# Performance work log

Hardware: AMD Instinct MI355X
Metric: run time of the kernel (lower is better)

## Reference

```python
import jax, jax.numpy as jnp
import numpy as np

H, W = 120, 160
FX, FY = 572.4114, 573.57043
CX, CY = 325.2611, 242.04899
CHUNK = 1200  # 19200 / 1200 = 16 scan steps
W_EDGE = 5.0
INV_SQRT_2PI = 1.0 / np.sqrt(2.0 * np.pi)


def backproject(depth):
    # depth: [H, W] -> organized cloud [H, W, 3]
    x = (jnp.arange(W, dtype=depth.dtype) - CX)[None, :]
    y = (jnp.arange(H, dtype=depth.dtype) - CY)[:, None]
    return jnp.stack((x * depth / FX, y * depth / FY, depth), axis=2)


def min_sq_dists(a, b):
    # For each point in a [N,3], squared distance to nearest point in b [M,3].
    # Tiled (flash-style) min-reduction: never materializes the full NxM matrix.
    b2 = jnp.sum(b * b, axis=-1)  # [M]
    n = a.shape[0]
    a_chunks = a.reshape(n // CHUNK, CHUNK, 3)

    def step(_, ac):
        a2 = jnp.sum(ac * ac, axis=-1)  # [chunk]
        d = a2[:, None] + b2[None, :] - 2.0 * (ac @ b.T)  # [chunk, M]
        return None, jnp.min(jnp.maximum(d, 0.0), axis=1)

    _, mins = jax.lax.scan(step, None, a_chunks)
    return mins.reshape(n)


def dilate(mask, ksize=9):
    # torch: clamp(conv2d(mask, ones(k,k), padding=k//2), 0, 1)
    k = jnp.ones((1, 1, ksize, ksize), mask.dtype)
    pad = ksize // 2
    out = jax.lax.conv_general_dilated(
        mask, k, window_strides=(1, 1), padding=[(pad, pad), (pad, pad)],
        dimension_numbers=("NCHW", "OIHW", "NCHW"))
    return jnp.clip(out, 0.0, 1.0)


def compute_mask_edge_weights(mask):
    # NOTE: original code calls mask_dilate_torch for BOTH dilate and erode
    # (a bug in the source), so mask_edge == 0 everywhere; replicated faithfully.
    dilated = dilate(mask, 9)
    eroded = dilate(mask, 9)
    mask_edge = dilated - eroded
    return jnp.exp(-0.5 * (mask_edge * W_EDGE) ** 2) * INV_SQRT_2PI + 1.0


def weighted_ex_loss_probs(probs, target, weight):
    pos = target > 0
    neg = target == 0
    p = jnp.clip(probs, 1e-7, 1.0 - 1e-7)
    pos_loss = jnp.where(pos, -target * jnp.log(p) * weight, 0.0)
    neg_loss = jnp.where(neg, -jnp.log(1.0 - p) * weight, 0.0)
    num_pos = jnp.sum(pos)
    num_neg = jnp.sum(neg)
    loss = jnp.where(num_pos > 0, jnp.sum(pos_loss) / jnp.maximum(num_pos, 1), 0.0)
    loss = loss + jnp.where(num_neg > 0, jnp.sum(neg_loss) / jnp.maximum(num_neg, 1), 0.0)
    return loss


def setup_inputs() -> dict:
    key = jax.random.key(0)
    k1, k2, k3, k4 = jax.random.split(key, 4)
    pred_PM = jax.random.uniform(k1, (1, H, W), dtype=jnp.float32)
    pred_Ms = (jax.random.uniform(k2, (1, H, W)) > 0.5).astype(jnp.float32)
    # strictly positive depths so the depth>0 mask keeps all H*W points (static shapes)
    depth_src = jax.random.uniform(k3, (H, W), dtype=jnp.float32) * 2.0 + 0.1
    depth_tgt = jax.random.uniform(k4, (H, W), dtype=jnp.float32) * 2.0 + 0.1
    return {"pred_PM": pred_PM, "pred_Ms": pred_Ms,
            "depth_src": depth_src, "depth_tgt": depth_tgt}


def reference(pred_PM, pred_Ms, depth_src, depth_tgt):
    # chamfer loss: backproject both depths, symmetric NN squared distance
    src_pts = backproject(depth_src).reshape(-1, 3)  # all z>0 by construction
    tgt_pts = backproject(depth_tgt).reshape(-1, 3)
    cham_loss = jnp.mean(min_sq_dists(src_pts, tgt_pts)) + jnp.mean(min_sq_dists(tgt_pts, src_pts))
    # mask loss: edge-weighted BCE-style loss
    p = pred_PM.reshape(-1, 1, H, W)
    m = pred_Ms.reshape(-1, 1, H, W)
    weights = compute_mask_edge_weights(m)
    mask_loss = weighted_ex_loss_probs(p, m, weights)
    return (cham_loss, mask_loss)
```

## Files before the change

### kernel.cpp

```cpp
#include <hip/hip_runtime.h>
#include <math.h>

#define HH 120
#define WW 160
#define NPTS (HH * WW)
#define FXC 572.4114f
#define FYC 573.57043f
#define CXC 325.2611f
#define CYC 242.04899f

#define CH_BT   64
#define CH_T    10
#define CH_APB  (CH_BT * CH_T)
#define CH_ABLK (NPTS / CH_APB)
#define CH_BTILE 192
#define CH_SCH  (NPTS / CH_BTILE)

#define MASK_WGT 1.3989422804014327f

#define GB_CH 64
#define GB_MK 16
#define GB_TOT (GB_CH + GB_MK)
#define CH_SEG (2 * NPTS / GB_CH)
#define MK_SEG (NPTS / GB_MK)

__device__ __forceinline__ void backproject_pt(int idx, float d,
                                               float& px, float& py, float& pz) {
    int y = idx / WW;
    int x = idx - y * WW;
    px = ((float)x - CXC) * d * (1.0f / FXC);
    py = ((float)y - CYC) * d * (1.0f / FYC);
    pz = d;
}

__device__ __forceinline__ float min3f(float a, float b, float c) {
    float d;
    asm("v_min3_f32 %0, %1, %2, %3" : "=v"(d) : "v"(a), "v"(b), "v"(c));
    return d;
}

__global__ void __launch_bounds__(256) init_k(int* __restrict__ mins,
                                              int* __restrict__ accs) {
    int i = blockIdx.x * 256 + threadIdx.x;
    if (i < 2 * NPTS) mins[i] = 0x7F800000;
    if (i < 6) accs[i] = 0;
}

__global__ void __launch_bounds__(CH_BT, 6) chamfer_partial_k(
    const float* __restrict__ depth_src, const float* __restrict__ depth_tgt,
    int* __restrict__ mins_base) {
    const float* dA;
    const float* dB;
    int* mins;
    if (blockIdx.z == 0) { dA = depth_src; dB = depth_tgt; mins = mins_base; }
    else                 { dA = depth_tgt; dB = depth_src; mins = mins_base + NPTS; }

    __shared__ float4 bp[CH_BTILE];

    const int tid = threadIdx.x;
    const int ablk = blockIdx.x;
    const int s = blockIdx.y;

#pragma unroll
    for (int r = 0; r < CH_BTILE / CH_BT; ++r) {
        int jj = r * CH_BT + tid;
        int j = s * CH_BTILE + jj;
        float d = dB[j];
        float px, py, pz;
        backproject_pt(j, d, px, py, pz);
        bp[jj] = make_float4(2.0f * px, 2.0f * py, 2.0f * pz,
                             fmaf(px, px, fmaf(py, py, pz * pz)));
    }

    float nax[CH_T], nay[CH_T], naz[CH_T], mn[CH_T];
#pragma unroll
    for (int t = 0; t < CH_T; ++t) {
        int i = ablk * CH_APB + t * CH_BT + tid;
        float d = dA[i];
        float px, py, pz;
        backproject_pt(i, d, px, py, pz);
        nax[t] = -px; nay[t] = -py; naz[t] = -pz;
        mn[t] = INFINITY;
    }

    __syncthreads();

    for (int jj = 0; jj < CH_BTILE; jj += 2) {
        float4 q0 = bp[jj + 0];
        float4 q1 = bp[jj + 1];
#pragma unroll
        for (int t = 0; t < CH_T; ++t) {
            float r0 = fmaf(nax[t], q0.x, fmaf(nay[t], q0.y, fmaf(naz[t], q0.z, q0.w)));
            float r1 = fmaf(nax[t], q1.x, fmaf(nay[t], q1.y, fmaf(naz[t], q1.z, q1.w)));
            mn[t] = min3f(mn[t], r0, r1);
        }
    }

#pragma unroll
    for (int t = 0; t < CH_T; ++t) {
        int i = ablk * CH_APB + t * CH_BT + tid;
        float a2 = fmaf(nax[t], nax[t], fmaf(nay[t], nay[t], naz[t] * naz[t]));
        float v = fmaxf(a2 + mn[t], 0.0f);
        atomicMin(&mins[i], __float_as_int(v));
    }
}

__global__ void __launch_bounds__(256) finalize_k(const int* __restrict__ mins,
                                                  const float* __restrict__ pm,
                                                  const float* __restrict__ ms,
                                                  float* __restrict__ accf,
                                                  int* __restrict__ acci,
                                                  float* __restrict__ out) {
    const int b = blockIdx.x;
    const int tid = threadIdx.x;
    __shared__ float ra[256], rb[256];
    __shared__ int ca[256], cb[256];

    if (b < GB_CH) {
        float s = 0.0f;
        int base = b * CH_SEG;
        for (int i = tid; i < CH_SEG; i += 256) s += __int_as_float(mins[base + i]);
        ra[tid] = s;
        __syncthreads();
        for (int w = 128; w > 0; w >>= 1) {
            if (tid < w) ra[tid] += ra[tid + w];
            __syncthreads();
        }
        if (tid == 0) atomicAdd(&accf[0], ra[0]);
    } else {
        int base = (b - GB_CH) * MK_SEG;
        float ps = 0.0f, ns = 0.0f;
        int pc = 0, nc = 0;
        for (int i = tid; i < MK_SEG; i += 256) {
            float p = pm[base + i];
            p = fminf(fmaxf(p, 1e-7f), 1.0f - 1e-7f);
            float t = ms[base + i];
            if (t > 0.0f) {
                ps += -t * logf(p) * MASK_WGT;
                pc++;
            } else if (t == 0.0f) {
                ns += -logf(1.0f - p) * MASK_WGT;
                nc++;
            }
        }
        ra[tid] = ps; rb[tid] = ns; ca[tid] = pc; cb[tid] = nc;
        __syncthreads();
        for (int w = 128; w > 0; w >>= 1) {
            if (tid < w) {
                ra[tid] += ra[tid + w];
                rb[tid] += rb[tid + w];
                ca[tid] += ca[tid + w];
                cb[tid] += cb[tid + w];
            }
            __syncthreads();
        }
        if (tid == 0) {
            atomicAdd(&accf[1], ra[0]);
            atomicAdd(&accf[2], rb[0]);
            atomicAdd(&acci[0], ca[0]);
            atomicAdd(&acci[1], cb[0]);
        }
    }

    if (tid == 0) {
        __threadfence();
        int old = __hip_atomic_fetch_add(&acci[2], 1, __ATOMIC_ACQ_REL,
                                         __HIP_MEMORY_SCOPE_AGENT);
        if (old == GB_TOT - 1) {
            __threadfence();
            float cham = __hip_atomic_load(&accf[0], __ATOMIC_RELAXED, __HIP_MEMORY_SCOPE_AGENT);
            float pos  = __hip_atomic_load(&accf[1], __ATOMIC_RELAXED, __HIP_MEMORY_SCOPE_AGENT);
            float neg  = __hip_atomic_load(&accf[2], __ATOMIC_RELAXED, __HIP_MEMORY_SCOPE_AGENT);
            int cp = __hip_atomic_load(&acci[0], __ATOMIC_RELAXED, __HIP_MEMORY_SCOPE_AGENT);
            int cn = __hip_atomic_load(&acci[1], __ATOMIC_RELAXED, __HIP_MEMORY_SCOPE_AGENT);
            out[0] = cham * (1.0f / (float)NPTS);
            float loss = 0.0f;
            if (cp > 0) loss += pos / (float)cp;
            if (cn > 0) loss += neg / (float)cn;
            out[1] = loss;
        }
    }
}

extern "C" void kernel_launch(void* const* d_in, const int* in_sizes, int n_in,
                              void* d_out, int out_size, void* d_ws, size_t ws_size,
                              hipStream_t stream) {
    const float* pred_PM   = (const float*)d_in[0];
    const float* pred_Ms   = (const float*)d_in[1];
    const float* depth_src = (const float*)d_in[2];
    const float* depth_tgt = (const float*)d_in[3];
    float* out = (float*)d_out;

    int* mins = (int*)d_ws;
    float* accf = (float*)(mins + 2 * NPTS);
    int* acci = (int*)(accf + 3);

    init_k<<<(2 * NPTS + 255) / 256, 256, 0, stream>>>(mins, (int*)accf);
    chamfer_partial_k<<<dim3(CH_ABLK, CH_SCH, 2), CH_BT, 0, stream>>>(
        depth_src, depth_tgt, mins);
    finalize_k<<<GB_TOT, 256, 0, stream>>>(mins, pred_PM, pred_Ms, accf, acci, out);
}
```

Measured before the change: 70.60 us.

## Enlarge chamfer blocks to 192 threads and software-prefetch LDS tile points

Raises the chamfer block size from 64 to 192 threads, so each block covers three times as many query points and each thread loads exactly one B-tile point into shared memory. The grid has a third as many A-blocks, which means fewer redundant tile backprojections and fewer blocks overall. The inner loop now prefetches the next pair of shared-memory points before computing on the current pair, to hide LDS latency. The trade-off is fewer total blocks, which may reduce occupancy and load balance on a GPU with many CUs, plus higher register pressure under launch_bounds(192, 8).

```diff
diff --git a/kernel.cpp b/kernel.cpp
--- a/kernel.cpp
+++ b/kernel.cpp
@@ -9,7 +9,7 @@
 #define CXC 325.2611f
 #define CYC 242.04899f
 
-#define CH_BT   64
+#define CH_BT   192
 #define CH_T    10
 #define CH_APB  (CH_BT * CH_T)
 #define CH_ABLK (NPTS / CH_APB)
@@ -46,7 +46,17 @@
     if (i < 6) accs[i] = 0;
 }
 
-__global__ void __launch_bounds__(CH_BT, 6) chamfer_partial_k(
+#define CH_BODY(Q0, Q1)                                                          \
+    _Pragma("unroll")                                                            \
+    for (int t = 0; t < CH_T; ++t) {                                             \
+        float r0 = fmaf(nax[t], (Q0).x,                                          \
+                        fmaf(nay[t], (Q0).y, fmaf(naz[t], (Q0).z, (Q0).w)));     \
+        float r1 = fmaf(nax[t], (Q1).x,                                          \
+                        fmaf(nay[t], (Q1).y, fmaf(naz[t], (Q1).z, (Q1).w)));     \
+        mn[t] = min3f(mn[t], r0, r1);                                            \
+    }
+
+__global__ void __launch_bounds__(CH_BT, 8) chamfer_partial_k(
     const float* __restrict__ depth_src, const float* __restrict__ depth_tgt,
     int* __restrict__ mins_base) {
     const float* dA;
@@ -61,15 +71,13 @@
     const int ablk = blockIdx.x;
     const int s = blockIdx.y;
 
-#pragma unroll
-    for (int r = 0; r < CH_BTILE / CH_BT; ++r) {
-        int jj = r * CH_BT + tid;
-        int j = s * CH_BTILE + jj;
+    {
+        int j = s * CH_BTILE + tid;
         float d = dB[j];
         float px, py, pz;
         backproject_pt(j, d, px, py, pz);
-        bp[jj] = make_float4(2.0f * px, 2.0f * py, 2.0f * pz,
-                             fmaf(px, px, fmaf(py, py, pz * pz)));
+        bp[tid] = make_float4(2.0f * px, 2.0f * py, 2.0f * pz,
+                              fmaf(px, px, fmaf(py, py, pz * pz)));
     }
 
     float nax[CH_T], nay[CH_T], naz[CH_T], mn[CH_T];
@@ -85,16 +93,16 @@
 
     __syncthreads();
 
-    for (int jj = 0; jj < CH_BTILE; jj += 2) {
-        float4 q0 = bp[jj + 0];
-        float4 q1 = bp[jj + 1];
-#pragma unroll
-        for (int t = 0; t < CH_T; ++t) {
-            float r0 = fmaf(nax[t], q0.x, fmaf(nay[t], q0.y, fmaf(naz[t], q0.z, q0.w)));
-            float r1 = fmaf(nax[t], q1.x, fmaf(nay[t], q1.y, fmaf(naz[t], q1.z, q1.w)));
-            mn[t] = min3f(mn[t], r0, r1);
-        }
-    }
+    float4 q0 = bp[0];
+    float4 q1 = bp[1];
+    for (int jj = 0; jj < CH_BTILE - 2; jj += 2) {
+        float4 n0 = bp[jj + 2];
+        float4 n1 = bp[jj + 3];
+        CH_BODY(q0, q1)
+        q0 = n0;
+        q1 = n1;
+    }
+    CH_BODY(q0, q1)
 
 #pragma unroll
     for (int t = 0; t < CH_T; ++t) {
```

New measurement: 81.31 us. +15.2%, slower.

## Precompute backprojected B points once and read them via scalar constant loads

Applied to the files above, without the earlier changes.

Backprojection of the B-side points now happens once in the init kernel, which writes float4 records to workspace. The chamfer kernel drops its per-block shared-memory tile and __syncthreads, and instead reads B points through an address_space(4) constant pointer, so the loads become uniform scalar loads. The block size is doubled to 128 threads with an occupancy hint of 8, which halves the number of A blocks. In exchange the chamfer kernel depends on scalar-cache bandwidth, and the workspace must grow to hold the precomputed points.

```diff
diff --git a/kernel.cpp b/kernel.cpp
--- a/kernel.cpp
+++ b/kernel.cpp
@@ -9,12 +9,12 @@
 #define CXC 325.2611f
 #define CYC 242.04899f
 
-#define CH_BT   64
+#define CH_BT   128
 #define CH_T    10
 #define CH_APB  (CH_BT * CH_T)
 #define CH_ABLK (NPTS / CH_APB)
-#define CH_BTILE 192
-#define CH_SCH  (NPTS / CH_BTILE)
+#define CH_CHUNK 192
+#define CH_SCH  (NPTS / CH_CHUNK)
 
 #define MASK_WGT 1.3989422804014327f
 
@@ -23,6 +23,9 @@
 #define GB_TOT (GB_CH + GB_MK)
 #define CH_SEG (2 * NPTS / GB_CH)
 #define MK_SEG (NPTS / GB_MK)
+
+typedef float __attribute__((ext_vector_type(4))) f4;
+typedef const __attribute__((address_space(4))) f4* cb4_t;
 
 __device__ __forceinline__ void backproject_pt(int idx, float d,
                                                float& px, float& py, float& pz) {
@@ -39,38 +42,38 @@
     return d;
 }
 
-__global__ void __launch_bounds__(256) init_k(int* __restrict__ mins,
+__global__ void __launch_bounds__(256) prep_k(const float* __restrict__ depth_src,
+                                              const float* __restrict__ depth_tgt,
+                                              f4* __restrict__ bp,
+                                              int* __restrict__ mins,
                                               int* __restrict__ accs) {
     int i = blockIdx.x * 256 + threadIdx.x;
-    if (i < 2 * NPTS) mins[i] = 0x7F800000;
+    if (i < 2 * NPTS) {
+        int dir = (i >= NPTS);
+        int idx = i - dir * NPTS;
+        float d = dir ? depth_tgt[idx] : depth_src[idx];
+        float px, py, pz;
+        backproject_pt(idx, d, px, py, pz);
+        f4 v = {2.0f * px, 2.0f * py, 2.0f * pz,
+                fmaf(px, px, fmaf(py, py, pz * pz))};
+        bp[i] = v;
+        mins[i] = 0x7F800000;
+    }
     if (i < 6) accs[i] = 0;
 }
 
-__global__ void __launch_bounds__(CH_BT, 6) chamfer_partial_k(
+__global__ void __launch_bounds__(CH_BT, 8) chamfer_k(
     const float* __restrict__ depth_src, const float* __restrict__ depth_tgt,
-    int* __restrict__ mins_base) {
+    const f4* __restrict__ bp, int* __restrict__ mins_base) {
     const float* dA;
-    const float* dB;
+    const f4* bB;
     int* mins;
-    if (blockIdx.z == 0) { dA = depth_src; dB = depth_tgt; mins = mins_base; }
-    else                 { dA = depth_tgt; dB = depth_src; mins = mins_base + NPTS; }
-
-    __shared__ float4 bp[CH_BTILE];
+    if (blockIdx.z == 0) { dA = depth_src; bB = bp + NPTS; mins = mins_base; }
+    else                 { dA = depth_tgt; bB = bp;        mins = mins_base + NPTS; }
 
     const int tid = threadIdx.x;
     const int ablk = blockIdx.x;
-    const int s = blockIdx.y;
-
-#pragma unroll
-    for (int r = 0; r < CH_BTILE / CH_BT; ++r) {
-        int jj = r * CH_BT + tid;
-        int j = s * CH_BTILE + jj;
-        float d = dB[j];
-        float px, py, pz;
-        backproject_pt(j, d, px, py, pz);
-        bp[jj] = make_float4(2.0f * px, 2.0f * py, 2.0f * pz,
-                             fmaf(px, px, fmaf(py, py, pz * pz)));
-    }
+    cb4_t B = (cb4_t)(bB + blockIdx.y * CH_CHUNK);
 
     float nax[CH_T], nay[CH_T], naz[CH_T], mn[CH_T];
 #pragma unroll
@@ -83,11 +86,10 @@
         mn[t] = INFINITY;
     }
 
-    __syncthreads();
-
-    for (int jj = 0; jj < CH_BTILE; jj += 2) {
-        float4 q0 = bp[jj + 0];
-        float4 q1 = bp[jj + 1];
+#pragma unroll 2
+    for (int j = 0; j < CH_CHUNK; j += 2) {
+        f4 q0 = B[j];
+        f4 q1 = B[j + 1];
 #pragma unroll
         for (int t = 0; t < CH_T; ++t) {
             float r0 = fmaf(nax[t], q0.x, fmaf(nay[t], q0.y, fmaf(naz[t], q0.z, q0.w)));
@@ -191,12 +193,14 @@
     const float* depth_tgt = (const float*)d_in[3];
     float* out = (float*)d_out;
 
-    int* mins = (int*)d_ws;
+    f4* bp = (f4*)d_ws;
+    int* mins = (int*)(bp + 2 * NPTS);
     float* accf = (float*)(mins + 2 * NPTS);
     int* acci = (int*)(accf + 3);
 
-    init_k<<<(2 * NPTS + 255) / 256, 256, 0, stream>>>(mins, (int*)accf);
-    chamfer_partial_k<<<dim3(CH_ABLK, CH_SCH, 2), CH_BT, 0, stream>>>(
-        depth_src, depth_tgt, mins);
+    prep_k<<<(2 * NPTS + 255) / 256, 256, 0, stream>>>(depth_src, depth_tgt,
+                                                       bp, mins, (int*)accf);
+    chamfer_k<<<dim3(CH_ABLK, CH_SCH, 2), CH_BT, 0, stream>>>(
+        depth_src, depth_tgt, bp, mins);
     finalize_k<<<GB_TOT, 256, 0, stream>>>(mins, pred_PM, pred_Ms, accf, acci, out);
 }
```

Measured after the change: 90.73 us. 28.5% more time.
